# Performance work log

Measured on AMD Instinct MI355X. Metric: run time of the kernel, lower is better.

Reference implementation:

```python
import jax, jax.numpy as jnp
import numpy as np

B, N, D, R = 32, 1024, 1152, 4


def setup_inputs() -> dict:
    key = jax.random.key(0)
    ks = jax.random.split(key, 9)
    s = 1.0 / np.sqrt(D)
    return {
        "x": jax.random.normal(ks[0], (B, N, D), dtype=jnp.float32),
        "Wq": jax.random.uniform(ks[1], (D, D), jnp.float32, -s, s),
        "bq": jax.random.uniform(ks[2], (D,), jnp.float32, -s, s),
        "Wk": jax.random.uniform(ks[3], (D, D), jnp.float32, -s, s),
        "bk": jax.random.uniform(ks[4], (D,), jnp.float32, -s, s),
        "Wv": jax.random.uniform(ks[5], (D, D), jnp.float32, -s, s),
        "bv": jax.random.uniform(ks[6], (D,), jnp.float32, -s, s),
        "Wo": jax.random.uniform(ks[7], (D, D), jnp.float32, -s, s),
        "bo": jax.random.uniform(ks[8], (D,), jnp.float32, -s, s),
        "r": R,
    }


def _merge(t, r):
    # VisionTokenMerger: non-overlapping window-mean over r consecutive tokens.
    b, n, d = t.shape
    merged = t.reshape(b, n // r, r, d).mean(axis=2)  # [B, N/r, D]
    return merged, r  # num_patches_per_token is the scalar window size


def reference(x, Wq, bq, Wk, bk, Wv, bv, Wo, bo, r):
    Q = x @ Wq.T + bq
    K = x @ Wk.T + bk
    V = x @ Wv.T + bv
    K_m, npt = _merge(K, r)            # [B, M, D], M = N/r
    V_m, _ = _merge(V, r)
    scale = 1.0 / jnp.sqrt(jnp.float32(Q.shape[-1]))
    scores = jnp.einsum('bnd,bmd->bnm', Q, K_m) * scale
    scores = scores + jnp.log(jnp.float32(npt))  # log-count additive bias
    w = jax.nn.softmax(scores, axis=-1)
    out = jnp.einsum('bnm,bmd->bnd', w, V_m)
    return out @ Wo.T + bo
```

## Files before the change

### kernel.cpp

```cpp
#include <hip/hip_runtime.h>
#include <hip/hip_bf16.h>


typedef __bf16 bf16;
typedef __attribute__((ext_vector_type(8))) __bf16 bf16x8;
typedef __attribute__((ext_vector_type(4))) __bf16 bf16x4;
typedef __attribute__((ext_vector_type(4))) float f32x4;

#define GAS __attribute__((address_space(1)))
#define LAS __attribute__((address_space(3)))

__device__ __forceinline__ void async_copy16(const void* g, void* s) {
    __builtin_amdgcn_global_load_lds((GAS unsigned int*)g, (LAS unsigned int*)s, 16, 0, 0);
}

template <typename OutT, bool HAS_BIAS>
__global__ __launch_bounds__(256) void gemm_bt(
    const bf16* __restrict__ A, const bf16* __restrict__ B,
    const float* __restrict__ bias, OutT* __restrict__ C,
    int N, int K, int lda, int ldb, int ldc, float scale,
    long sAb, long sBb, long sCb) {
    __shared__ __align__(16) bf16 As[128 * 32];
    __shared__ __align__(16) bf16 Bs[128 * 32];
    const int tid  = threadIdx.x;
    const int wave = tid >> 6;
    const int lane = tid & 63;
    const int quad = lane >> 4;
    const int l16  = lane & 15;
    const int wM   = (wave >> 1) * 64;
    const int wN   = (wave & 1) * 64;

    int bx = blockIdx.x, by = blockIdx.y;
    const int nbx = gridDim.x, nby = gridDim.y;
    if (((nby & 7) == 0) && (nbx % 9 == 0)) {
        int lid = by * nbx + bx;
        int xcd = lid & 7;
        int s   = lid >> 3;
        int Pn  = nby >> 3;
        int gsz = 9 * Pn;
        int g   = s / gsz;
        int rem = s - g * gsz;
        int p   = rem / 9;
        by = p * 8 + xcd;
        bx = g * 9 + (rem - p * 9);
    }

    const long zb = blockIdx.z;
    A += zb * sAb;
    B += zb * sBb;
    C += zb * sCb;

    const int rowBase = by * 128;
    const int colBase = bx * 128;

    const int g0 = wave * 64 + lane;
    const int r0 = g0 >> 2;
    const int c0 = (g0 & 3) * 8;
    const bf16* a0 = A + (long)(rowBase + r0) * lda + c0;
    const bf16* a1 = A + (long)(rowBase + 64 + r0) * lda + c0;
    const bf16* b0 = B + (long)(colBase + r0) * ldb + c0;
    const bf16* b1 = B + (long)(colBase + 64 + r0) * ldb + c0;
    char* lA0 = (char*)As + wave * 1024;
    char* lA1 = (char*)As + 4096 + wave * 1024;
    char* lB0 = (char*)Bs + wave * 1024;
    char* lB1 = (char*)Bs + 4096 + wave * 1024;

    f32x4 acc[4][4] = {};

    const int kt = K >> 5;
    for (int k = 0; k < kt; ++k) {
        __syncthreads();
        async_copy16(a0, lA0);
        async_copy16(a1, lA1);
        async_copy16(b0, lB0);
        async_copy16(b1, lB1);
        a0 += 32; a1 += 32; b0 += 32; b1 += 32;
        __syncthreads();
        bf16x8 af[4], bfv[4];
#pragma unroll
        for (int t = 0; t < 4; ++t) {
            af[t]  = *(const bf16x8*)(As + (wM + t * 16 + l16) * 32 + quad * 8);
            bfv[t] = *(const bf16x8*)(Bs + (wN + t * 16 + l16) * 32 + quad * 8);
        }
#pragma unroll
        for (int mt = 0; mt < 4; ++mt)
#pragma unroll
            for (int nt = 0; nt < 4; ++nt)
                acc[mt][nt] = __builtin_amdgcn_mfma_f32_16x16x32_bf16(
                    af[mt], bfv[nt], acc[mt][nt], 0, 0, 0);
    }

#pragma unroll
    for (int mt = 0; mt < 4; ++mt) {
        const int row = rowBase + wM + mt * 16 + quad * 4;
#pragma unroll
        for (int nt = 0; nt < 4; ++nt) {
            const int col = colBase + wN + nt * 16 + l16;
            const float bv = HAS_BIAS ? bias[col] : 0.0f;
#pragma unroll
            for (int r = 0; r < 4; ++r) {
                float v = acc[mt][nt][r] * scale + bv;
                C[(long)(row + r) * ldc + col] = (OutT)v;
            }
        }
    }
}

__global__ __launch_bounds__(512) void scores_softmax_k(
    const bf16* __restrict__ X, const bf16* __restrict__ UVW,
    const float* __restrict__ cvec, bf16* __restrict__ P) {
    __shared__ __align__(16) bf16 As[128 * 32];
    __shared__ __align__(16) bf16 Bs[256 * 32];
    __shared__ float red[128][4];
    __shared__ float red2[128][4];
    const int tid  = threadIdx.x;
    const int wave = tid >> 6;
    const int lane = tid & 63;
    const int quad = lane >> 4;
    const int l16  = lane & 15;
    const int wM   = (wave >> 2) * 64;
    const int wN   = (wave & 3) * 64;
    const int wc   = wave & 3;

    int bx = blockIdx.x, by = blockIdx.y;
    {
        int lid = by * 8 + bx;
        int xcd = lid & 7;
        int s   = lid >> 3;
        by = (s >> 3) * 8 + xcd;
        bx = s & 7;
    }
    const long b = by;
    const bf16* A = X + (b * 1024 + (long)bx * 128) * 1152;
    const bf16* B = UVW + b * 256 * 2304;

    const int ra = tid >> 2, ca = (tid & 3) * 8;
    const bf16* a0 = A + (long)ra * 1152 + ca;
    const bf16* b0 = B + (long)ra * 2304 + ca;
    const bf16* b1 = B + (long)(128 + ra) * 2304 + ca;
    char* lA  = (char*)As + wave * 1024;
    char* lB0 = (char*)Bs + wave * 1024;
    char* lB1 = (char*)Bs + 8192 + wave * 1024;

    f32x4 acc[4][4] = {};
#pragma unroll 1
    for (int k = 0; k < 36; ++k) {
        __syncthreads();
        async_copy16(a0, lA);
        async_copy16(b0, lB0);
        async_copy16(b1, lB1);
        a0 += 32; b0 += 32; b1 += 32;
        __syncthreads();
        bf16x8 af[4], bfv[4];
#pragma unroll
        for (int t = 0; t < 4; ++t) {
            af[t]  = *(const bf16x8*)(As + (wM + t * 16 + l16) * 32 + quad * 8);
            bfv[t] = *(const bf16x8*)(Bs + (wN + t * 16 + l16) * 32 + quad * 8);
        }
#pragma unroll
        for (int mt = 0; mt < 4; ++mt)
#pragma unroll
            for (int nt = 0; nt < 4; ++nt)
                acc[mt][nt] = __builtin_amdgcn_mfma_f32_16x16x32_bf16(
                    af[mt], bfv[nt], acc[mt][nt], 0, 0, 0);
    }

    float cv[4];
#pragma unroll
    for (int nt = 0; nt < 4; ++nt) cv[nt] = cvec[b * 256 + wN + nt * 16 + l16];
#pragma unroll
    for (int mt = 0; mt < 4; ++mt)
#pragma unroll
        for (int nt = 0; nt < 4; ++nt)
#pragma unroll
            for (int r = 0; r < 4; ++r) acc[mt][nt][r] += cv[nt];

    const float scale = 0.029462782549439484f;

#pragma unroll
    for (int mt = 0; mt < 4; ++mt)
#pragma unroll
        for (int r = 0; r < 4; ++r) {
            float pm = fmaxf(fmaxf(acc[mt][0][r], acc[mt][1][r]),
                             fmaxf(acc[mt][2][r], acc[mt][3][r]));
#pragma unroll
            for (int off = 1; off <= 8; off <<= 1) pm = fmaxf(pm, __shfl_xor(pm, off));
            if (l16 == 0) red[wM + mt * 16 + quad * 4 + r][wc] = pm;
        }
    __syncthreads();
#pragma unroll
    for (int mt = 0; mt < 4; ++mt)
#pragma unroll
        for (int r = 0; r < 4; ++r) {
            const int R = wM + mt * 16 + quad * 4 + r;
            float4 q = *(const float4*)red[R];
            float m = fmaxf(fmaxf(q.x, q.y), fmaxf(q.z, q.w));
            float ps = 0.0f;
#pragma unroll
            for (int nt = 0; nt < 4; ++nt) {
                float e = __expf((acc[mt][nt][r] - m) * scale);
                acc[mt][nt][r] = e;
                ps += e;
            }
#pragma unroll
            for (int off = 1; off <= 8; off <<= 1) ps += __shfl_xor(ps, off);
            if (l16 == 0) red2[R][wc] = ps;
        }
    __syncthreads();
#pragma unroll
    for (int mt = 0; mt < 4; ++mt)
#pragma unroll
        for (int r = 0; r < 4; ++r) {
            const int R = wM + mt * 16 + quad * 4 + r;
            float4 q = *(const float4*)red2[R];
            float inv = 1.0f / (q.x + q.y + q.z + q.w);
            const long gr = b * 1024 + (long)bx * 128 + R;
#pragma unroll
            for (int nt = 0; nt < 4; ++nt)
                P[gr * 256 + wN + nt * 16 + l16] = (bf16)(acc[mt][nt][r] * inv);
        }
}

__global__ void cvt_wT_k(const float* __restrict__ Wq, const float* __restrict__ Wk,
                         const float* __restrict__ Wv, bf16* __restrict__ dst) {
    __shared__ bf16 t[64][66];
    const int z = blockIdx.z;
    const float* src = z == 0 ? Wq : z == 1 ? Wk : Wv;
    bf16* d = dst + (long)(z == 0 ? 0 : z == 1 ? 2 : 3) * 1327104;
    const int r0 = blockIdx.y * 64, c0 = blockIdx.x * 64;
    const int tid = threadIdx.x;
    {
        int row = tid >> 4;
        int col4 = (tid & 15) * 4;
#pragma unroll
        for (int p = 0; p < 4; ++p) {
            int r = row + p * 16;
            float4 v = *(const float4*)(src + (long)(r0 + r) * 1152 + c0 + col4);
            t[col4 + 0][r] = (bf16)v.x;
            t[col4 + 1][r] = (bf16)v.y;
            t[col4 + 2][r] = (bf16)v.z;
            t[col4 + 3][r] = (bf16)v.w;
        }
    }
    __syncthreads();
    {
        int orow = tid >> 2;
        int oc = (tid & 3) * 16;
        bf16x8 a, b2;
#pragma unroll
        for (int j = 0; j < 8; ++j) { a[j] = t[orow][oc + j]; b2[j] = t[orow][oc + 8 + j]; }
        bf16* o = d + (long)(c0 + orow) * 1152 + r0 + oc;
        *(bf16x8*)o = a;
        *(bf16x8*)(o + 8) = b2;
    }
}

__global__ void cvt_w_plain_k(const float* __restrict__ Wo, bf16* __restrict__ dst) {
    int i = blockIdx.x * 256 + threadIdx.x;
    float4 v = ((const float4*)Wo)[i];
    bf16x4 o = {(bf16)v.x, (bf16)v.y, (bf16)v.z, (bf16)v.w};
    ((bf16x4*)(dst + 1327104))[i] = o;
}

__global__ void cvt_merge_x_k(const float* __restrict__ x, bf16* __restrict__ xb,
                              bf16* __restrict__ xm) {
    int i = blockIdx.x * 256 + threadIdx.x;
    int w = i / 288;
    int c4 = i - w * 288;
    const float4* p = (const float4*)(x + (long)w * 4608) + c4;
    float4 a = p[0], b = p[288], c = p[576], d = p[864];
    bf16x4 oa = {(bf16)a.x, (bf16)a.y, (bf16)a.z, (bf16)a.w};
    bf16x4 ob = {(bf16)b.x, (bf16)b.y, (bf16)b.z, (bf16)b.w};
    bf16x4 oc = {(bf16)c.x, (bf16)c.y, (bf16)c.z, (bf16)c.w};
    bf16x4 od = {(bf16)d.x, (bf16)d.y, (bf16)d.z, (bf16)d.w};
    bf16* base = xb + (long)w * 4608 + c4 * 4;
    *(bf16x4*)(base)        = oa;
    *(bf16x4*)(base + 1152) = ob;
    *(bf16x4*)(base + 2304) = oc;
    *(bf16x4*)(base + 3456) = od;
    float4 s;
    s.x = (a.x + b.x + c.x + d.x) * 0.25f;
    s.y = (a.y + b.y + c.y + d.y) * 0.25f;
    s.z = (a.z + b.z + c.z + d.z) * 0.25f;
    s.w = (a.w + b.w + c.w + d.w) * 0.25f;
    bf16x4 o = {(bf16)s.x, (bf16)s.y, (bf16)s.z, (bf16)s.w};
    *(bf16x4*)(xm + (long)w * 1152 + c4 * 4) = o;
}

__global__ void rowdot_k(const bf16* __restrict__ M, const float* __restrict__ v,
                         float* __restrict__ out, float* __restrict__ z) {
    const int row = blockIdx.x * 4 + (threadIdx.x >> 6);
    const int lane = threadIdx.x & 63;
    const bf16* mr = M + (long)row * 1152;
    float acc = 0.0f;
#pragma unroll
    for (int j = 0; j < 18; ++j)
        acc += (float)mr[j * 64 + lane] * v[j * 64 + lane];
#pragma unroll
    for (int off = 32; off; off >>= 1) acc += __shfl_xor(acc, off, 64);
    if (lane == 0) {
        out[row] = acc;
        if (z) z[row] = 0.0f;
    }
}

__global__ void transpose_vm_k(const bf16* __restrict__ UVW, bf16* __restrict__ VT) {
    __shared__ bf16 t[64][65];
    const int tid = threadIdx.x;
    const int b = blockIdx.z;
    const int d0 = blockIdx.x * 64, m0 = blockIdx.y * 64;
#pragma unroll
    for (int p = 0; p < 2; ++p) {
        int r = (tid >> 3) + p * 32;
        int c = (tid & 7) * 8;
        bf16x8 v = *(const bf16x8*)(UVW + (long)(b * 256 + m0 + r) * 2304 + 1152 + d0 + c);
#pragma unroll
        for (int j = 0; j < 8; ++j) t[c + j][r] = v[j];
    }
    __syncthreads();
#pragma unroll
    for (int p = 0; p < 2; ++p) {
        int r = (tid >> 3) + p * 32;
        int c = (tid & 7) * 8;
        bf16x8 o;
#pragma unroll
        for (int j = 0; j < 8; ++j) o[j] = t[r][c + j];
        *(bf16x8*)(VT + (long)b * 294912 + (long)(d0 + r) * 256 + m0 + c) = o;
    }
}

extern "C" void kernel_launch(void* const* d_in, const int* in_sizes, int n_in,
                              void* d_out, int out_size, void* d_ws, size_t ws_size,
                              hipStream_t stream) {
    const float* x  = (const float*)d_in[0];
    const float* Wq = (const float*)d_in[1];
    const float* bq = (const float*)d_in[2];
    const float* Wk = (const float*)d_in[3];
    const float* bk = (const float*)d_in[4];  (void)bk;
    const float* Wv = (const float*)d_in[5];
    const float* bv = (const float*)d_in[6];
    const float* Wo = (const float*)d_in[7];
    const float* bo = (const float*)d_in[8];
    float* out = (float*)d_out;
    char* ws = (char*)d_ws;

    bf16* WT4    = (bf16*)(ws);
    bf16* WkT_b  = WT4 + 2 * 1327104;
    bf16* Wo_b   = WT4 + 1 * 1327104;
    bf16* WQK2   = (bf16*)(ws + 10616832);
    float* biasUV = (float*)(ws + 15925248);
    float* vk     = (float*)(ws + 15934464);
    float* cvec   = (float*)(ws + 15939072);
    bf16* xm_b   = (bf16*)(ws + 15971840);
    bf16* UVW    = (bf16*)(ws + 34846208);
    bf16* VWT    = (bf16*)(ws + 72594944);
    bf16* P_b    = (bf16*)(ws + 91469312);

    bf16* x_b = (bf16*)d_out;

    cvt_wT_k<<<dim3(18, 18, 3), 256, 0, stream>>>(Wq, Wk, Wv, WT4);
    cvt_w_plain_k<<<1296, 256, 0, stream>>>(Wo, WT4);
    cvt_merge_x_k<<<9216, 256, 0, stream>>>(x, x_b, xm_b);

    gemm_bt<bf16, false><<<dim3(9, 9, 2), 256, 0, stream>>>(
        WT4, WT4 + 2 * 1327104, nullptr, WQK2,
        1152, 1152, 1152, 1152, 1152, 1.0f, 1327104, 1327104, 1327104);

    rowdot_k<<<288, 256, 0, stream>>>(WkT_b, bq, vk, biasUV);
    rowdot_k<<<288, 256, 0, stream>>>(Wo_b, bv, biasUV + 1152, nullptr);

    gemm_bt<bf16, true><<<dim3(18, 64, 1), 256, 0, stream>>>(
        xm_b, WQK2, biasUV, UVW, 2304, 1152, 1152, 1152, 2304, 1.0f, 0, 0, 0);

    rowdot_k<<<2048, 256, 0, stream>>>(xm_b, vk, cvec, nullptr);

    transpose_vm_k<<<dim3(18, 4, 32), 256, 0, stream>>>(UVW, VWT);

    scores_softmax_k<<<dim3(8, 32), 512, 0, stream>>>(x_b, UVW, cvec, P_b);

    gemm_bt<float, true><<<dim3(9, 8, 32), 256, 0, stream>>>(
        P_b, VWT, bo, out, 1152, 256, 256, 256, 1152, 1.0f,
        1024L * 256, 1152L * 256, 1024L * 1152);
}
```

Baseline: 500.6 us.

## Fuse scores-softmax with the PV output GEMM and merge small launches

Scores, softmax and the final P·VWᵀ GEMM now run in one kernel. Each block holds its normalized probability tile in shared memory and loops over output column chunks, so the bf16 P matrix is no longer written to and read back from global memory. The weight conversion kernels and the two bias rowdot kernels are merged into single launches, and workspace and output buffers are reassigned to match. Tiles shrink to 64 rows with 256 threads, so the grid has more blocks. The cost is that each block reloads the full VWT slice and now runs a long serial GEMM loop with more syncs.

```diff
diff --git a/kernel.cpp b/kernel.cpp
--- a/kernel.cpp
+++ b/kernel.cpp
@@ -106,55 +106,55 @@
     }
 }
 
-__global__ __launch_bounds__(512) void scores_softmax_k(
+__global__ __launch_bounds__(256) void fused_attn_k(
     const bf16* __restrict__ X, const bf16* __restrict__ UVW,
-    const float* __restrict__ cvec, bf16* __restrict__ P) {
-    __shared__ __align__(16) bf16 As[128 * 32];
+    const bf16* __restrict__ VWT, const float* __restrict__ cvec,
+    const float* __restrict__ bo, float* __restrict__ out) {
+    __shared__ __align__(16) bf16 As[64 * 32];
     __shared__ __align__(16) bf16 Bs[256 * 32];
-    __shared__ float red[128][4];
-    __shared__ float red2[128][4];
+    __shared__ __align__(16) bf16 Ps[64][264];
+    __shared__ float red[64][4];
+    __shared__ float red2[64][4];
     const int tid  = threadIdx.x;
     const int wave = tid >> 6;
     const int lane = tid & 63;
     const int quad = lane >> 4;
     const int l16  = lane & 15;
-    const int wM   = (wave >> 2) * 64;
-    const int wN   = (wave & 3) * 64;
-    const int wc   = wave & 3;
+    const int wN   = wave * 64;
 
     int bx = blockIdx.x, by = blockIdx.y;
     {
-        int lid = by * 8 + bx;
+        int lid = by * 16 + bx;
         int xcd = lid & 7;
         int s   = lid >> 3;
-        by = (s >> 3) * 8 + xcd;
-        bx = s & 7;
+        by = (s >> 4) * 8 + xcd;
+        bx = s & 15;
     }
     const long b = by;
-    const bf16* A = X + (b * 1024 + (long)bx * 128) * 1152;
-    const bf16* B = UVW + b * 256 * 2304;
+    const bf16* Abase = X + (b * 1024 + (long)bx * 64) * 1152;
+    const bf16* Bbase = UVW + b * 256 * 2304;
 
     const int ra = tid >> 2, ca = (tid & 3) * 8;
-    const bf16* a0 = A + (long)ra * 1152 + ca;
-    const bf16* b0 = B + (long)ra * 2304 + ca;
-    const bf16* b1 = B + (long)(128 + ra) * 2304 + ca;
-    char* lA  = (char*)As + wave * 1024;
-    char* lB0 = (char*)Bs + wave * 1024;
-    char* lB1 = (char*)Bs + 8192 + wave * 1024;
+    const bf16* aptr = Abase + (long)ra * 1152 + ca;
+    const bf16* bptr = Bbase + (long)ra * 2304 + ca;
+    char* lA = (char*)As + wave * 1024;
+    char* lB = (char*)Bs + wave * 1024;
 
     f32x4 acc[4][4] = {};
 #pragma unroll 1
     for (int k = 0; k < 36; ++k) {
         __syncthreads();
-        async_copy16(a0, lA);
-        async_copy16(b0, lB0);
-        async_copy16(b1, lB1);
-        a0 += 32; b0 += 32; b1 += 32;
+        async_copy16(aptr, lA);
+        async_copy16(bptr,               lB);
+        async_copy16(bptr +  64 * 2304,  lB + 4096);
+        async_copy16(bptr + 128 * 2304,  lB + 8192);
+        async_copy16(bptr + 192 * 2304,  lB + 12288);
+        aptr += 32; bptr += 32;
         __syncthreads();
         bf16x8 af[4], bfv[4];
 #pragma unroll
         for (int t = 0; t < 4; ++t) {
-            af[t]  = *(const bf16x8*)(As + (wM + t * 16 + l16) * 32 + quad * 8);
+            af[t]  = *(const bf16x8*)(As + (t * 16 + l16) * 32 + quad * 8);
             bfv[t] = *(const bf16x8*)(Bs + (wN + t * 16 + l16) * 32 + quad * 8);
         }
 #pragma unroll
@@ -185,14 +185,14 @@
                              fmaxf(acc[mt][2][r], acc[mt][3][r]));
 #pragma unroll
             for (int off = 1; off <= 8; off <<= 1) pm = fmaxf(pm, __shfl_xor(pm, off));
-            if (l16 == 0) red[wM + mt * 16 + quad * 4 + r][wc] = pm;
+            if (l16 == 0) red[mt * 16 + quad * 4 + r][wave] = pm;
         }
     __syncthreads();
 #pragma unroll
     for (int mt = 0; mt < 4; ++mt)
 #pragma unroll
         for (int r = 0; r < 4; ++r) {
-            const int R = wM + mt * 16 + quad * 4 + r;
+            const int R = mt * 16 + quad * 4 + r;
             float4 q = *(const float4*)red[R];
             float m = fmaxf(fmaxf(q.x, q.y), fmaxf(q.z, q.w));
             float ps = 0.0f;
@@ -204,31 +204,87 @@
             }
 #pragma unroll
             for (int off = 1; off <= 8; off <<= 1) ps += __shfl_xor(ps, off);
-            if (l16 == 0) red2[R][wc] = ps;
+            if (l16 == 0) red2[R][wave] = ps;
         }
     __syncthreads();
 #pragma unroll
     for (int mt = 0; mt < 4; ++mt)
 #pragma unroll
         for (int r = 0; r < 4; ++r) {
-            const int R = wM + mt * 16 + quad * 4 + r;
+            const int R = mt * 16 + quad * 4 + r;
             float4 q = *(const float4*)red2[R];
             float inv = 1.0f / (q.x + q.y + q.z + q.w);
-            const long gr = b * 1024 + (long)bx * 128 + R;
 #pragma unroll
             for (int nt = 0; nt < 4; ++nt)
-                P[gr * 256 + wN + nt * 16 + l16] = (bf16)(acc[mt][nt][r] * inv);
-        }
-}
-
-__global__ void cvt_wT_k(const float* __restrict__ Wq, const float* __restrict__ Wk,
-                         const float* __restrict__ Wv, bf16* __restrict__ dst) {
+                Ps[R][wN + nt * 16 + l16] = (bf16)(acc[mt][nt][r] * inv);
+        }
+
+    const bf16* VWTb = VWT + b * 294912;
+    const int wRow  = (wave >> 1) * 32;
+    const int wCol2 = (wave & 1) * 64;
+    const int rb2 = tid >> 2, cb2 = (tid & 3) * 8;
+    const long orow0 = b * 1024 + bx * 64;
+
+#pragma unroll 1
+    for (int d0 = 0; d0 < 1152; d0 += 128) {
+        f32x4 acc2[2][4] = {};
+#pragma unroll 1
+        for (int kk = 0; kk < 256; kk += 32) {
+            __syncthreads();
+            async_copy16(VWTb + (long)(d0 + rb2) * 256 + kk + cb2,
+                         (char*)Bs + wave * 1024);
+            async_copy16(VWTb + (long)(d0 + 64 + rb2) * 256 + kk + cb2,
+                         (char*)Bs + 4096 + wave * 1024);
+            __syncthreads();
+            bf16x8 af2[2], bf2[4];
+#pragma unroll
+            for (int t = 0; t < 2; ++t)
+                af2[t] = *(const bf16x8*)&Ps[wRow + t * 16 + l16][kk + quad * 8];
+#pragma unroll
+            for (int t = 0; t < 4; ++t)
+                bf2[t] = *(const bf16x8*)(Bs + (wCol2 + t * 16 + l16) * 32 + quad * 8);
+#pragma unroll
+            for (int mt = 0; mt < 2; ++mt)
+#pragma unroll
+                for (int nt = 0; nt < 4; ++nt)
+                    acc2[mt][nt] = __builtin_amdgcn_mfma_f32_16x16x32_bf16(
+                        af2[mt], bf2[nt], acc2[mt][nt], 0, 0, 0);
+        }
+#pragma unroll
+        for (int mt = 0; mt < 2; ++mt) {
+            const long row = orow0 + wRow + mt * 16 + quad * 4;
+#pragma unroll
+            for (int nt = 0; nt < 4; ++nt) {
+                const int col = d0 + wCol2 + nt * 16 + l16;
+                const float bb = bo[col];
+#pragma unroll
+                for (int r = 0; r < 4; ++r)
+                    out[(row + r) * 1152 + col] = acc2[mt][nt][r] + bb;
+            }
+        }
+    }
+}
+
+__global__ void cvt_w_k(const float* __restrict__ Wq, const float* __restrict__ Wk,
+                        const float* __restrict__ Wv, const float* __restrict__ Wo,
+                        bf16* __restrict__ dst) {
+    const int z = blockIdx.z;
+    const int tid = threadIdx.x;
+    if (z == 3) {
+        long i0 = ((long)(blockIdx.y * 18 + blockIdx.x) * 256 + tid) * 4;
+        bf16* d = dst + 1327104;
+#pragma unroll
+        for (int p = 0; p < 4; ++p) {
+            float4 v = ((const float4*)Wo)[i0 + p];
+            bf16x4 o = {(bf16)v.x, (bf16)v.y, (bf16)v.z, (bf16)v.w};
+            ((bf16x4*)d)[i0 + p] = o;
+        }
+        return;
+    }
     __shared__ bf16 t[64][66];
-    const int z = blockIdx.z;
     const float* src = z == 0 ? Wq : z == 1 ? Wk : Wv;
     bf16* d = dst + (long)(z == 0 ? 0 : z == 1 ? 2 : 3) * 1327104;
     const int r0 = blockIdx.y * 64, c0 = blockIdx.x * 64;
-    const int tid = threadIdx.x;
     {
         int row = tid >> 4;
         int col4 = (tid & 15) * 4;
@@ -255,11 +311,38 @@
     }
 }
 
-__global__ void cvt_w_plain_k(const float* __restrict__ Wo, bf16* __restrict__ dst) {
-    int i = blockIdx.x * 256 + threadIdx.x;
-    float4 v = ((const float4*)Wo)[i];
-    bf16x4 o = {(bf16)v.x, (bf16)v.y, (bf16)v.z, (bf16)v.w};
-    ((bf16x4*)(dst + 1327104))[i] = o;
+__global__ void rowdot2_k(const bf16* __restrict__ WkT, const bf16* __restrict__ Wo,
+                          const float* __restrict__ bq, const float* __restrict__ bv,
+                          float* __restrict__ vk, float* __restrict__ biasUV) {
+    const int row = blockIdx.x * 4 + (threadIdx.x >> 6);
+    const int lane = threadIdx.x & 63;
+    const bf16* M = blockIdx.y == 0 ? WkT : Wo;
+    const float* v = blockIdx.y == 0 ? bq : bv;
+    const bf16* mr = M + (long)row * 1152;
+    float acc = 0.0f;
+#pragma unroll
+    for (int j = 0; j < 18; ++j)
+        acc += (float)mr[j * 64 + lane] * v[j * 64 + lane];
+#pragma unroll
+    for (int off = 32; off; off >>= 1) acc += __shfl_xor(acc, off, 64);
+    if (lane == 0) {
+        if (blockIdx.y == 0) { vk[row] = acc; biasUV[row] = 0.0f; }
+        else biasUV[1152 + row] = acc;
+    }
+}
+
+__global__ void rowdot_k(const bf16* __restrict__ M, const float* __restrict__ v,
+                         float* __restrict__ out) {
+    const int row = blockIdx.x * 4 + (threadIdx.x >> 6);
+    const int lane = threadIdx.x & 63;
+    const bf16* mr = M + (long)row * 1152;
+    float acc = 0.0f;
+#pragma unroll
+    for (int j = 0; j < 18; ++j)
+        acc += (float)mr[j * 64 + lane] * v[j * 64 + lane];
+#pragma unroll
+    for (int off = 32; off; off >>= 1) acc += __shfl_xor(acc, off, 64);
+    if (lane == 0) out[row] = acc;
 }
 
 __global__ void cvt_merge_x_k(const float* __restrict__ x, bf16* __restrict__ xb,
@@ -287,23 +370,6 @@
     *(bf16x4*)(xm + (long)w * 1152 + c4 * 4) = o;
 }
 
-__global__ void rowdot_k(const bf16* __restrict__ M, const float* __restrict__ v,
-                         float* __restrict__ out, float* __restrict__ z) {
-    const int row = blockIdx.x * 4 + (threadIdx.x >> 6);
-    const int lane = threadIdx.x & 63;
-    const bf16* mr = M + (long)row * 1152;
-    float acc = 0.0f;
-#pragma unroll
-    for (int j = 0; j < 18; ++j)
-        acc += (float)mr[j * 64 + lane] * v[j * 64 + lane];
-#pragma unroll
-    for (int off = 32; off; off >>= 1) acc += __shfl_xor(acc, off, 64);
-    if (lane == 0) {
-        out[row] = acc;
-        if (z) z[row] = 0.0f;
-    }
-}
-
 __global__ void transpose_vm_k(const bf16* __restrict__ UVW, bf16* __restrict__ VT) {
     __shared__ bf16 t[64][65];
     const int tid = threadIdx.x;
@@ -344,41 +410,35 @@
     float* out = (float*)d_out;
     char* ws = (char*)d_ws;
 
-    bf16* WT4    = (bf16*)(ws);
-    bf16* WkT_b  = WT4 + 2 * 1327104;
-    bf16* Wo_b   = WT4 + 1 * 1327104;
-    bf16* WQK2   = (bf16*)(ws + 10616832);
-    float* biasUV = (float*)(ws + 15925248);
-    float* vk     = (float*)(ws + 15934464);
-    float* cvec   = (float*)(ws + 15939072);
-    bf16* xm_b   = (bf16*)(ws + 15971840);
-    bf16* UVW    = (bf16*)(ws + 34846208);
-    bf16* VWT    = (bf16*)(ws + 72594944);
-    bf16* P_b    = (bf16*)(ws + 91469312);
-
-    bf16* x_b = (bf16*)d_out;
-
-    cvt_wT_k<<<dim3(18, 18, 3), 256, 0, stream>>>(Wq, Wk, Wv, WT4);
-    cvt_w_plain_k<<<1296, 256, 0, stream>>>(Wo, WT4);
+    bf16* WT4   = (bf16*)ws;
+    bf16* WkT_b = WT4 + 2 * 1327104;
+    bf16* Wo_b  = WT4 + 1 * 1327104;
+    bf16* x_b   = (bf16*)ws;
+    bf16* WQK2  = (bf16*)(ws + 75497472);
+    float* biasUV = (float*)(ws + 80805888);
+    float* vk     = (float*)(ws + 80815104);
+    float* cvec   = (float*)(ws + 80819712);
+    bf16* UVW   = (bf16*)(ws + 80852480);
+    bf16* VWT   = (bf16*)(ws + 118601216);
+
+    bf16* xm_b = (bf16*)d_out;
+
+    cvt_w_k<<<dim3(18, 18, 4), 256, 0, stream>>>(Wq, Wk, Wv, Wo, WT4);
+
+    gemm_bt<bf16, false><<<dim3(9, 9, 2), 256, 0, stream>>>(
+        WT4, WkT_b, nullptr, WQK2,
+        1152, 1152, 1152, 1152, 1152, 1.0f, 1327104, 1327104, 1327104);
+
+    rowdot2_k<<<dim3(288, 2), 256, 0, stream>>>(WkT_b, Wo_b, bq, bv, vk, biasUV);
+
     cvt_merge_x_k<<<9216, 256, 0, stream>>>(x, x_b, xm_b);
-
-    gemm_bt<bf16, false><<<dim3(9, 9, 2), 256, 0, stream>>>(
-        WT4, WT4 + 2 * 1327104, nullptr, WQK2,
-        1152, 1152, 1152, 1152, 1152, 1.0f, 1327104, 1327104, 1327104);
-
-    rowdot_k<<<288, 256, 0, stream>>>(WkT_b, bq, vk, biasUV);
-    rowdot_k<<<288, 256, 0, stream>>>(Wo_b, bv, biasUV + 1152, nullptr);
 
     gemm_bt<bf16, true><<<dim3(18, 64, 1), 256, 0, stream>>>(
         xm_b, WQK2, biasUV, UVW, 2304, 1152, 1152, 1152, 2304, 1.0f, 0, 0, 0);
 
-    rowdot_k<<<2048, 256, 0, stream>>>(xm_b, vk, cvec, nullptr);
+    rowdot_k<<<2048, 256, 0, stream>>>(xm_b, vk, cvec);
 
     transpose_vm_k<<<dim3(18, 4, 32), 256, 0, stream>>>(UVW, VWT);
 
-    scores_softmax_k<<<dim3(8, 32), 512, 0, stream>>>(x_b, UVW, cvec, P_b);
-
-    gemm_bt<float, true><<<dim3(9, 8, 32), 256, 0, stream>>>(
-        P_b, VWT, bo, out, 1152, 256, 256, 256, 1152, 1.0f,
-        1024L * 256, 1152L * 256, 1024L * 1152);
-}
+    fused_attn_k<<<dim3(16, 32), 256, 0, stream>>>(x_b, UVW, VWT, cvec, bo, out);
+}
```

New measurement: 501.7 us. No clear change (+0.2%).
